# Kernel tuning notes

Hardware: AMD Instinct MI355X
Metric: run time of the kernel (lower is better)

## Reference

```python
import jax, jax.numpy as jnp
import numpy as np

T, B = 256, 512
IMG_FLAT = 25          # 5*5*num_channels
FEAT = 16; LOC = 4; EMB = 4
LSTM_IN = FEAT + LOC + EMB  # 24
H = 128
GRID = 10.0


def _lin(k, out_d, in_d, scale=0.05):
    kw, kb = jax.random.split(k)
    return (jax.random.normal(kw, (out_d, in_d), jnp.float32) * scale,
            jax.random.normal(kb, (out_d,), jnp.float32) * scale)


def setup_inputs() -> dict:
    key = jax.random.key(0)
    ks = jax.random.split(key, 16)
    image = jax.random.uniform(ks[0], (T * B, 5, 5), jnp.float32) * 255.0
    location = jax.random.uniform(ks[1], (T * B, 2), jnp.float32) * GRID
    message = jax.random.normal(ks[2], (T * B, 1), jnp.float32)
    done = jax.random.randint(ks[3], (T * B,), 0, 2, jnp.int32)
    h0 = jnp.zeros((1, B, H), jnp.float32)
    c0 = jnp.zeros((1, B, H), jnp.float32)
    Wv1, bv1 = _lin(ks[4], 256, IMG_FLAT)
    Wv2, bv2 = _lin(ks[5], 256, 256)
    Wv3, bv3 = _lin(ks[6], 128, 256)
    Wv4, bv4 = _lin(ks[7], FEAT, 128)
    Wl, bl = _lin(ks[8], LOC, 2)
    Wm, bm = _lin(ks[9], EMB, 1)
    Wih, bih = _lin(ks[10], 4 * H, LSTM_IN)
    Whh, bhh = _lin(ks[11], 4 * H, H)
    return dict(image=image, location=location, message=message, done=done,
                h0=h0, c0=c0,
                Wv1=Wv1, bv1=bv1, Wv2=Wv2, bv2=bv2, Wv3=Wv3, bv3=bv3,
                Wv4=Wv4, bv4=bv4, Wl=Wl, bl=bl, Wm=Wm, bm=bm,
                Wih=Wih, bih=bih, Whh=Whh, bhh=bhh)


def _get_states(image, location, message, done_f, h0, c0,
                Wv1, bv1, Wv2, bv2, Wv3, bv3, Wv4, bv4,
                Wl, bl, Wm, bm, Wih, bih, Whh, bhh):
    batch = h0.shape[1]
    # encoders (all rows at once, faithful to torch version)
    x = image.reshape(image.shape[0], -1) / 255.0
    f = jax.nn.relu(x @ Wv1.T + bv1)
    f = jax.nn.relu(f @ Wv2.T + bv2)
    f = jax.nn.relu(f @ Wv3.T + bv3)
    image_feat = jax.nn.relu(f @ Wv4.T + bv4)                  # [TB, 16]
    loc_feat = (location / GRID) @ Wl.T + bl                    # [TB, 4]
    msg = (1.0 - done_f)[:, None] * message
    msg_feat = jax.nn.relu(msg @ Wm.T + bm)                     # [TB, 4]
    hid = jnp.concatenate([image_feat, loc_feat, msg_feat], axis=1)
    hid = hid.reshape(-1, batch, LSTM_IN)                       # [T, B, 24]
    d_seq = done_f.reshape(-1, batch)                           # [T, B]

    def step(carry, xd):
        h, c = carry
        x_t, d_t = xd
        mask = (1.0 - d_t)[:, None]
        h = h * mask
        c = c * mask
        gates = x_t @ Wih.T + bih + h @ Whh.T + bhh             # [B, 4H]
        i, fg, g, o = jnp.split(gates, 4, axis=-1)
        c = jax.nn.sigmoid(fg) * c + jax.nn.sigmoid(i) * jnp.tanh(g)
        h = jax.nn.sigmoid(o) * jnp.tanh(c)
        return (h, c), h

    (hT, cT), hs = jax.lax.scan(step, (h0[0], c0[0]), (hid, d_seq))
    new_hidden = hs.reshape(-1, H)                              # [TB, 128]
    return new_hidden, hT[None], cT[None]


def reference(image, location, message, done, h0, c0,
              Wv1, bv1, Wv2, bv2, Wv3, bv3, Wv4, bv4,
              Wl, bl, Wm, bm, Wih, bih, Whh, bhh):
    done_f = done.astype(jnp.float32)
    return _get_states(image, location, message, done_f, h0, c0,
                       Wv1, bv1, Wv2, bv2, Wv3, bv3, Wv4, bv4,
                       Wl, bl, Wm, bm, Wih, bih, Whh, bhh)
```

## Files before the change

### kernel.cpp

```cpp
#include <hip/hip_runtime.h>
#include <hip/hip_bf16.h>

#define T_STEPS 256
#define BATCH   512
#define HID     128
#define TBROWS  (T_STEPS * BATCH)
#define XH_STRIDE 32

typedef short  bh8   __attribute__((ext_vector_type(8)));
typedef _Float16 h8  __attribute__((ext_vector_type(8)));
typedef float  f32x4 __attribute__((ext_vector_type(4)));

__device__ __forceinline__ unsigned short f2bf_bits(float x) {
    union { float f; unsigned int u; } a; a.f = x;
    unsigned int r = a.u + 0x7fffu + ((a.u >> 16) & 1u);
    return (unsigned short)(r >> 16);
}
__device__ __forceinline__ unsigned short f2h_bits(float x) {
    union { _Float16 h; unsigned short u; } z; z.h = (_Float16)x; return z.u;
}
__device__ __forceinline__ unsigned int pack2h(float a, float b) {
    union { _Float16 h[2]; unsigned int u; } z;
    z.h[0] = (_Float16)a; z.h[1] = (_Float16)b; return z.u;
}
__device__ __forceinline__ unsigned int pack2bf(float a, float b) {
    return (unsigned int)f2bf_bits(a) | ((unsigned int)f2bf_bits(b) << 16);
}

#if __has_builtin(__builtin_amdgcn_rcpf)
__device__ __forceinline__ float frcp(float x) { return __builtin_amdgcn_rcpf(x); }
#else
__device__ __forceinline__ float frcp(float x) { return 1.0f / x; }
#endif
#if __has_builtin(__builtin_amdgcn_exp2f)
__device__ __forceinline__ float fexp2(float x) { return __builtin_amdgcn_exp2f(x); }
#else
__device__ __forceinline__ float fexp2(float x) { return __expf(x * 0.6931471806f); }
#endif
#define LOG2E 1.442695041f
__device__ __forceinline__ float sigf(float x) {
    return frcp(1.0f + fexp2(-x * LOG2E));
}
__device__ __forceinline__ float tanh_fast(float x) {
    return fmaf(-2.0f, frcp(1.0f + fexp2(x * (2.0f * LOG2E))), 1.0f);
}

__device__ __forceinline__ float swz16(float v) {
    return __int_as_float(
        __builtin_amdgcn_ds_swizzle(__float_as_int(v), 0x000F));
}

__device__ __forceinline__ void barrier_lds_only() {
    asm volatile("s_waitcnt lgkmcnt(0)" ::: "memory");
    __builtin_amdgcn_s_barrier();
    asm volatile("" ::: "memory");
}

__device__ __forceinline__ void fragstore(unsigned short* dst, const float* W,
                                          int i, int NT, int Kreal) {
    const int j    = i & 7;
    const int lane = (i >> 3) & 63;
    const int ts   = i >> 9;
    const int nt   = ts % NT;
    const int ks   = ts / NT;
    const int n = nt * 16 + (lane & 15);
    const int k = ks * 32 + (lane >> 4) * 8 + j;
    dst[i] = (k < Kreal) ? f2bf_bits(W[n * Kreal + k]) : (unsigned short)0;
}

#define NE1 8192
#define NE2 65536
#define NE3 32768
#define NE4 2048
#define NWC 81920
#define NBS 512
#define PREP_TOTAL (NE1 + NE2 + NE3 + NE4 + NWC + NBS)

__global__ __launch_bounds__(256) void prep_kernel(
    const float* __restrict__ W1, const float* __restrict__ W2,
    const float* __restrict__ W3, const float* __restrict__ W4,
    const float* __restrict__ Wih, const float* __restrict__ bih,
    const float* __restrict__ Whh, const float* __restrict__ bhh,
    unsigned short* __restrict__ w1f, unsigned short* __restrict__ w2f,
    unsigned short* __restrict__ w3f, unsigned short* __restrict__ w4f,
    unsigned short* __restrict__ wcf, float* __restrict__ bsum)
{
    int i = blockIdx.x * 256 + threadIdx.x;
    if (i < NE1) { fragstore(w1f, W1, i, 16, 25); return; }
    i -= NE1;
    if (i < NE2) { fragstore(w2f, W2, i, 16, 256); return; }
    i -= NE2;
    if (i < NE3) { fragstore(w3f, W3, i, 8, 256); return; }
    i -= NE3;
    if (i < NE4) { fragstore(w4f, W4, i, 1, 128); return; }
    i -= NE4;
    if (i < NWC) {
        const int j    = i & 7;
        const int lane = (i >> 3) & 63;
        const int ts   = i >> 9;
        const int mt   = ts / 5;
        const int kt   = ts - mt * 5;
        const int m = mt * 16 + (lane & 15);
        const int k = kt * 32 + (lane >> 4) * 8 + j;
        float v = 0.0f;
        if (k < 128)      v = Whh[m * 128 + k];
        else if (k < 152) v = Wih[m * 24 + (k - 128)];
        wcf[i] = f2h_bits(v);
        return;
    }
    i -= NWC;
    if (i < NBS) bsum[i] = bih[i] + bhh[i];
}

#define ASTRIDE 264
#define ESAMP 64

__global__ __launch_bounds__(256) void encoder_kernel(
    const float* __restrict__ img,
    const float* __restrict__ loc,
    const float* __restrict__ msg,
    const int*   __restrict__ done,
    const float* __restrict__ B1, const float* __restrict__ B2,
    const float* __restrict__ B3, const float* __restrict__ B4,
    const float* __restrict__ Wl, const float* __restrict__ Bl,
    const float* __restrict__ Wm, const float* __restrict__ Bm,
    const unsigned short* __restrict__ w1f, const unsigned short* __restrict__ w2f,
    const unsigned short* __restrict__ w3f, const unsigned short* __restrict__ w4f,
    unsigned short* __restrict__ xcat_h)
{
    __shared__ __align__(16) unsigned short actA[ESAMP][ASTRIDE];
    __shared__ __align__(16) unsigned short actB[ESAMP][ASTRIDE];

    const int tid  = threadIdx.x;
    const int w    = tid >> 6;
    const int lane = tid & 63;
    const int n    = lane & 15;
    const int quad = lane >> 4;
    const int row0 = blockIdx.x * ESAMP;

    if (tid < ESAMP) {
        const int grow = row0 + tid;
        const float l0 = loc[(size_t)grow * 2 + 0] * 0.1f;
        const float l1 = loc[(size_t)grow * 2 + 1] * 0.1f;
        #pragma unroll
        for (int c = 0; c < 4; ++c)
            xcat_h[(size_t)grow * XH_STRIDE + 16 + c] =
                f2h_bits(fmaf(Wl[c * 2 + 0], l0, fmaf(Wl[c * 2 + 1], l1, Bl[c])));
        const float mm = (1.0f - (float)done[grow]) * msg[grow];
        #pragma unroll
        for (int c = 0; c < 4; ++c)
            xcat_h[(size_t)grow * XH_STRIDE + 20 + c] =
                f2h_bits(fmaxf(fmaf(Wm[c], mm, Bm[c]), 0.0f));
    }

    const f32x4 zero4 = {0.0f, 0.0f, 0.0f, 0.0f};

    {
        bh8 bimg[4];
        #pragma unroll
        for (int sg = 0; sg < 4; ++sg) {
            const size_t grow = row0 + sg * 16 + n;
            #pragma unroll
            for (int j = 0; j < 8; ++j) {
                const int k = quad * 8 + j;
                const float v = (k < 25) ? img[grow * 25 + k] * (1.0f / 255.0f) : 0.0f;
                bimg[sg][j] = (short)f2bf_bits(v);
            }
        }
        #pragma unroll
        for (int mt = 0; mt < 4; ++mt) {
            const int mtg = w * 4 + mt;
            const bh8 a = *reinterpret_cast<const bh8*>(w1f + (size_t)(mtg * 64 + lane) * 8);
            f32x4 acc[4];
            #pragma unroll
            for (int sg = 0; sg < 4; ++sg)
                acc[sg] = __builtin_amdgcn_mfma_f32_16x16x32_bf16(a, bimg[sg], zero4, 0, 0, 0);
            const float4 bv = *reinterpret_cast<const float4*>(B1 + mtg * 16 + quad * 4);
            #pragma unroll
            for (int sg = 0; sg < 4; ++sg) {
                const float v0 = fmaxf(acc[sg][0] + bv.x, 0.0f);
                const float v1 = fmaxf(acc[sg][1] + bv.y, 0.0f);
                const float v2 = fmaxf(acc[sg][2] + bv.z, 0.0f);
                const float v3 = fmaxf(acc[sg][3] + bv.w, 0.0f);
                uint2 pk; pk.x = pack2bf(v0, v1); pk.y = pack2bf(v2, v3);
                *reinterpret_cast<uint2*>(&actA[sg * 16 + n][mtg * 16 + quad * 4]) = pk;
            }
        }
    }
    __syncthreads();

    {
        f32x4 a2[4][4];
        #pragma unroll
        for (int mt = 0; mt < 4; ++mt)
            #pragma unroll
            for (int sg = 0; sg < 4; ++sg) a2[mt][sg] = zero4;
        #pragma unroll
        for (int kt = 0; kt < 8; ++kt) {
            bh8 b[4];
            #pragma unroll
            for (int sg = 0; sg < 4; ++sg)
                b[sg] = *reinterpret_cast<const bh8*>(&actA[sg * 16 + n][kt * 32 + quad * 8]);
            #pragma unroll
            for (int mt = 0; mt < 4; ++mt) {
                const int mtg = w * 4 + mt;
                const bh8 a = *reinterpret_cast<const bh8*>(
                    w2f + (size_t)((kt * 16 + mtg) * 64 + lane) * 8);
                #pragma unroll
                for (int sg = 0; sg < 4; ++sg)
                    a2[mt][sg] = __builtin_amdgcn_mfma_f32_16x16x32_bf16(a, b[sg], a2[mt][sg], 0, 0, 0);
            }
        }
        #pragma unroll
        for (int mt = 0; mt < 4; ++mt) {
            const int mtg = w * 4 + mt;
            const float4 bv = *reinterpret_cast<const float4*>(B2 + mtg * 16 + quad * 4);
            #pragma unroll
            for (int sg = 0; sg < 4; ++sg) {
                const float v0 = fmaxf(a2[mt][sg][0] + bv.x, 0.0f);
                const float v1 = fmaxf(a2[mt][sg][1] + bv.y, 0.0f);
                const float v2 = fmaxf(a2[mt][sg][2] + bv.z, 0.0f);
                const float v3 = fmaxf(a2[mt][sg][3] + bv.w, 0.0f);
                uint2 pk; pk.x = pack2bf(v0, v1); pk.y = pack2bf(v2, v3);
                *reinterpret_cast<uint2*>(&actB[sg * 16 + n][mtg * 16 + quad * 4]) = pk;
            }
        }
    }
    __syncthreads();

    {
        f32x4 a3[2][4];
        #pragma unroll
        for (int mt = 0; mt < 2; ++mt)
            #pragma unroll
            for (int sg = 0; sg < 4; ++sg) a3[mt][sg] = zero4;
        #pragma unroll
        for (int kt = 0; kt < 8; ++kt) {
            bh8 b[4];
            #pragma unroll
            for (int sg = 0; sg < 4; ++sg)
                b[sg] = *reinterpret_cast<const bh8*>(&actB[sg * 16 + n][kt * 32 + quad * 8]);
            #pragma unroll
            for (int mt = 0; mt < 2; ++mt) {
                const int mtg = w * 2 + mt;
                const bh8 a = *reinterpret_cast<const bh8*>(
                    w3f + (size_t)((kt * 8 + mtg) * 64 + lane) * 8);
                #pragma unroll
                for (int sg = 0; sg < 4; ++sg)
                    a3[mt][sg] = __builtin_amdgcn_mfma_f32_16x16x32_bf16(a, b[sg], a3[mt][sg], 0, 0, 0);
            }
        }
        #pragma unroll
        for (int mt = 0; mt < 2; ++mt) {
            const int mtg = w * 2 + mt;
            const float4 bv = *reinterpret_cast<const float4*>(B3 + mtg * 16 + quad * 4);
            #pragma unroll
            for (int sg = 0; sg < 4; ++sg) {
                const float v0 = fmaxf(a3[mt][sg][0] + bv.x, 0.0f);
                const float v1 = fmaxf(a3[mt][sg][1] + bv.y, 0.0f);
                const float v2 = fmaxf(a3[mt][sg][2] + bv.z, 0.0f);
                const float v3 = fmaxf(a3[mt][sg][3] + bv.w, 0.0f);
                uint2 pk; pk.x = pack2bf(v0, v1); pk.y = pack2bf(v2, v3);
                *reinterpret_cast<uint2*>(&actA[sg * 16 + n][mtg * 16 + quad * 4]) = pk;
            }
        }
    }
    __syncthreads();

    {
        f32x4 a4 = zero4;
        #pragma unroll
        for (int kt = 0; kt < 4; ++kt) {
            const bh8 b = *reinterpret_cast<const bh8*>(&actA[w * 16 + n][kt * 32 + quad * 8]);
            const bh8 a = *reinterpret_cast<const bh8*>(w4f + (size_t)(kt * 64 + lane) * 8);
            a4 = __builtin_amdgcn_mfma_f32_16x16x32_bf16(a, b, a4, 0, 0, 0);
        }
        const float4 bv = *reinterpret_cast<const float4*>(B4 + quad * 4);
        const int grow = row0 + w * 16 + n;
        const float v0 = fmaxf(a4[0] + bv.x, 0.0f);
        const float v1 = fmaxf(a4[1] + bv.y, 0.0f);
        const float v2 = fmaxf(a4[2] + bv.z, 0.0f);
        const float v3 = fmaxf(a4[3] + bv.w, 0.0f);
        uint2 pk; pk.x = pack2h(v0, v1); pk.y = pack2h(v2, v3);
        *reinterpret_cast<uint2*>(xcat_h + (size_t)grow * XH_STRIDE + quad * 4) = pk;
    }
}

#define COLS 2

__global__ __launch_bounds__(512) void lstm_kernel(
    const unsigned short* __restrict__ xcat_h,
    const int*   __restrict__ done,
    const float* __restrict__ h0,
    const float* __restrict__ c0,
    const unsigned short* __restrict__ wcf,
    const float* __restrict__ bsum,
    float* __restrict__ out)
{
    __shared__ __align__(16) unsigned short xls[T_STEPS][COLS][32];
    __shared__ __align__(16) unsigned short hx[2][COLS][HID];
    __shared__ int dls[T_STEPS][COLS];

    const int tid  = threadIdx.x;
    const int w    = tid >> 6;
    const int lane = tid & 63;
    const int n    = lane & 15;
    const int quad = lane >> 4;
    const int bb   = blockIdx.x * COLS;

    for (int i = tid; i < T_STEPS * COLS * 16; i += 512) {
        const int dw = i & 15;
        const int rc = i >> 4;
        const int st = rc >> 1, cl = rc & 1;
        unsigned int v = 0u;
        if (dw < 12)
            v = *reinterpret_cast<const unsigned int*>(
                xcat_h + (size_t)(st * BATCH + bb + cl) * XH_STRIDE + dw * 2);
        *reinterpret_cast<unsigned int*>(&xls[st][cl][dw * 2]) = v;
    }
    if (tid < T_STEPS * COLS) {
        const int st = tid >> 1, cl = tid & 1;
        dls[st][cl] = done[st * BATCH + bb + cl];
    }

    h8 wf[4][5];
    #pragma unroll
    for (int g = 0; g < 4; ++g)
        #pragma unroll
        for (int kt = 0; kt < 5; ++kt)
            wf[g][kt] = *reinterpret_cast<const h8*>(
                wcf + (size_t)(((g * 8 + w) * 5 + kt) * 64 + lane) * 8);

    const int unit = w * 16 + n;
    f32x4 bini[4];
    #pragma unroll
    for (int g = 0; g < 4; ++g) {
        const float b = bsum[g * 128 + unit];
        bini[g] = (f32x4){b, b, b, b};
    }

    const bool owner = (lane < 32);
    const int col = quad & 1;

    float c_ = 0.0f, h0v = 0.0f;
    if (owner) {
        c_  = c0[(size_t)(bb + col) * HID + unit];
        h0v = h0[(size_t)(bb + col) * HID + unit];
    }
    __syncthreads();

    if (owner)
        hx[0][col][unit] = f2h_bits(h0v * (1.0f - (float)dls[0][col]));
    __syncthreads();

    float hl = 0.0f;

    h8 bf[5];
    #pragma unroll
    for (int kt = 0; kt < 5; ++kt) bf[kt] = (h8)(_Float16)0.0f;

    #pragma unroll 1
    for (int s = 0; s < T_STEPS; ++s) {
        const int buf = s & 1;

        if (n < COLS) {
            #pragma unroll
            for (int kt = 0; kt < 4; ++kt)
                bf[kt] = *reinterpret_cast<const h8*>(&hx[buf][n][kt * 32 + quad * 8]);
            bf[4] = *reinterpret_cast<const h8*>(&xls[s][n][quad * 8]);
        }

        const int sn = (s + 1 < T_STEPS) ? s + 1 : T_STEPS - 1;
        const int m_cur = dls[s][col];
        const int m_nxt = dls[sn][col];

        f32x4 acc[4];
        #pragma unroll
        for (int g = 0; g < 4; ++g) acc[g] = bini[g];
        #pragma unroll
        for (int kt = 0; kt < 5; ++kt)
            #pragma unroll
            for (int g = 0; g < 4; ++g)
                acc[g] = __builtin_amdgcn_mfma_f32_16x16x32_f16(
                    bf[kt], wf[g][kt], acc[g], 0, 0, 0);

        float g4[4];
        #pragma unroll
        for (int g = 0; g < 4; ++g) {
            const float t0 = swz16(acc[g][0]);
            const float t1 = swz16(acc[g][1]);
            g4[g] = (lane & 16) ? t1 : t0;
        }

        if (owner) {
            const float cn = sigf(g4[1]) * (c_ * (1.0f - (float)m_cur))
                           + sigf(g4[0]) * tanh_fast(g4[2]);
            const float hn = sigf(g4[3]) * tanh_fast(cn);
            c_ = cn; hl = hn;
            out[(size_t)(s * BATCH + bb + col) * HID + unit] = hn;
            hx[buf ^ 1][col][unit] = f2h_bits(hn * (1.0f - (float)m_nxt));
        }
        barrier_lds_only();
    }

    const size_t base = (size_t)TBROWS * HID;
    if (owner) {
        out[base + (size_t)(bb + col) * HID + unit] = hl;
        out[base + (size_t)BATCH * HID + (size_t)(bb + col) * HID + unit] = c_;
    }
}

extern "C" void kernel_launch(void* const* d_in, const int* in_sizes, int n_in,
                              void* d_out, int out_size, void* d_ws, size_t ws_size,
                              hipStream_t stream) {
    const float* img  = (const float*)d_in[0];
    const float* loc  = (const float*)d_in[1];
    const float* msg  = (const float*)d_in[2];
    const int*   done = (const int*)d_in[3];
    const float* h0   = (const float*)d_in[4];
    const float* c0   = (const float*)d_in[5];
    const float* W1   = (const float*)d_in[6];
    const float* B1   = (const float*)d_in[7];
    const float* W2   = (const float*)d_in[8];
    const float* B2   = (const float*)d_in[9];
    const float* W3   = (const float*)d_in[10];
    const float* B3   = (const float*)d_in[11];
    const float* W4   = (const float*)d_in[12];
    const float* B4   = (const float*)d_in[13];
    const float* Wl   = (const float*)d_in[14];
    const float* Bl   = (const float*)d_in[15];
    const float* Wm   = (const float*)d_in[16];
    const float* Bm   = (const float*)d_in[17];
    const float* Wih  = (const float*)d_in[18];
    const float* bih  = (const float*)d_in[19];
    const float* Whh  = (const float*)d_in[20];
    const float* bhh  = (const float*)d_in[21];

    char* wsb = (char*)d_ws;
    unsigned short* xcat_h = (unsigned short*)wsb;
    unsigned short* w1f = (unsigned short*)(wsb + (size_t)TBROWS * XH_STRIDE * 2);
    unsigned short* w2f = w1f + NE1;
    unsigned short* w3f = w2f + NE2;
    unsigned short* w4f = w3f + NE3;
    unsigned short* wcf = w4f + NE4;
    float*          bsum = (float*)(wcf + NWC);

    float* out = (float*)d_out;

    prep_kernel<<<(PREP_TOTAL + 255) / 256, 256, 0, stream>>>(
        W1, W2, W3, W4, Wih, bih, Whh, bhh,
        w1f, w2f, w3f, w4f, wcf, bsum);
    encoder_kernel<<<TBROWS / ESAMP, 256, 0, stream>>>(
        img, loc, msg, done, B1, B2, B3, B4, Wl, Bl, Wm, Bm,
        w1f, w2f, w3f, w4f, xcat_h);
    lstm_kernel<<<BATCH / COLS, 512, 0, stream>>>(
        xcat_h, done, h0, c0, wcf, bsum, out);
}
```

Baseline: 344.4 us.

## Make encoder persistent over 8 tiles with register-resident weights and prefetch

The encoder now runs 512-thread blocks that each process 8 tiles of 64 rows. Every wave loads its MFMA weight fragments and biases into registers once, instead of re-reading them from global memory for each 64-row tile. The biases are folded into the accumulator initialisation, and the next tile's image data is prefetched while the current tile computes. The cost is much higher register pressure (launch bounds 512,2), an extra barrier per tile and fewer blocks in the grid. Wave 4 and above sit idle in the last layer.

```diff
diff --git a/kernel.cpp b/kernel.cpp
--- a/kernel.cpp
+++ b/kernel.cpp
@@ -113,9 +113,134 @@
 }
 
 #define ASTRIDE 264
-#define ESAMP 64
-
-__global__ __launch_bounds__(256) void encoder_kernel(
+#define ETILES 8
+#define EBLK   512
+
+__device__ __forceinline__ void enc_tile(
+    const float* __restrict__ img, unsigned short* __restrict__ xcat_h,
+    unsigned short (*bufA)[ASTRIDE], unsigned short (*bufB)[ASTRIDE],
+    const bh8 (&wf1)[2], const bh8 (&wf2)[8][2], const bh8 (&wf3)[8],
+    const bh8 (&wf4)[4],
+    const f32x4 (&bi1)[2], const f32x4 (&bi2)[2], const f32x4& bi3,
+    const f32x4& bi4,
+    float (&fin)[4][8], float (&fnx)[4][8],
+    int row0, int nrow0, bool pf, int w, int n, int quad)
+{
+    bh8 bimg[4];
+    #pragma unroll
+    for (int sg = 0; sg < 4; ++sg)
+        #pragma unroll
+        for (int j = 0; j < 8; ++j)
+            bimg[sg][j] = (short)f2bf_bits(fin[sg][j] * (1.0f / 255.0f));
+
+    if (pf) {
+        #pragma unroll
+        for (int sg = 0; sg < 4; ++sg) {
+            const size_t grow = (size_t)(nrow0 + sg * 16 + n);
+            #pragma unroll
+            for (int j = 0; j < 8; ++j) {
+                const int k = quad * 8 + j;
+                fnx[sg][j] = (k < 25) ? img[grow * 25 + k] : 0.0f;
+            }
+        }
+    }
+
+    #pragma unroll
+    for (int mt = 0; mt < 2; ++mt) {
+        f32x4 acc[4];
+        #pragma unroll
+        for (int sg = 0; sg < 4; ++sg)
+            acc[sg] = __builtin_amdgcn_mfma_f32_16x16x32_bf16(
+                wf1[mt], bimg[sg], bi1[mt], 0, 0, 0);
+        #pragma unroll
+        for (int sg = 0; sg < 4; ++sg) {
+            uint2 pk;
+            pk.x = pack2bf(fmaxf(acc[sg][0], 0.0f), fmaxf(acc[sg][1], 0.0f));
+            pk.y = pack2bf(fmaxf(acc[sg][2], 0.0f), fmaxf(acc[sg][3], 0.0f));
+            *reinterpret_cast<uint2*>(
+                &bufA[sg * 16 + n][(2 * w + mt) * 16 + quad * 4]) = pk;
+        }
+    }
+    barrier_lds_only();
+
+    {
+        f32x4 a2[2][4];
+        #pragma unroll
+        for (int mt = 0; mt < 2; ++mt)
+            #pragma unroll
+            for (int sg = 0; sg < 4; ++sg) a2[mt][sg] = bi2[mt];
+        #pragma unroll
+        for (int kt = 0; kt < 8; ++kt) {
+            bh8 b[4];
+            #pragma unroll
+            for (int sg = 0; sg < 4; ++sg)
+                b[sg] = *reinterpret_cast<const bh8*>(
+                    &bufA[sg * 16 + n][kt * 32 + quad * 8]);
+            #pragma unroll
+            for (int mt = 0; mt < 2; ++mt)
+                #pragma unroll
+                for (int sg = 0; sg < 4; ++sg)
+                    a2[mt][sg] = __builtin_amdgcn_mfma_f32_16x16x32_bf16(
+                        wf2[kt][mt], b[sg], a2[mt][sg], 0, 0, 0);
+        }
+        #pragma unroll
+        for (int mt = 0; mt < 2; ++mt)
+            #pragma unroll
+            for (int sg = 0; sg < 4; ++sg) {
+                uint2 pk;
+                pk.x = pack2bf(fmaxf(a2[mt][sg][0], 0.0f), fmaxf(a2[mt][sg][1], 0.0f));
+                pk.y = pack2bf(fmaxf(a2[mt][sg][2], 0.0f), fmaxf(a2[mt][sg][3], 0.0f));
+                *reinterpret_cast<uint2*>(
+                    &bufB[sg * 16 + n][(2 * w + mt) * 16 + quad * 4]) = pk;
+            }
+    }
+    barrier_lds_only();
+
+    {
+        f32x4 a3[4];
+        #pragma unroll
+        for (int sg = 0; sg < 4; ++sg) a3[sg] = bi3;
+        #pragma unroll
+        for (int kt = 0; kt < 8; ++kt) {
+            bh8 b[4];
+            #pragma unroll
+            for (int sg = 0; sg < 4; ++sg)
+                b[sg] = *reinterpret_cast<const bh8*>(
+                    &bufB[sg * 16 + n][kt * 32 + quad * 8]);
+            #pragma unroll
+            for (int sg = 0; sg < 4; ++sg)
+                a3[sg] = __builtin_amdgcn_mfma_f32_16x16x32_bf16(
+                    wf3[kt], b[sg], a3[sg], 0, 0, 0);
+        }
+        #pragma unroll
+        for (int sg = 0; sg < 4; ++sg) {
+            uint2 pk;
+            pk.x = pack2bf(fmaxf(a3[sg][0], 0.0f), fmaxf(a3[sg][1], 0.0f));
+            pk.y = pack2bf(fmaxf(a3[sg][2], 0.0f), fmaxf(a3[sg][3], 0.0f));
+            *reinterpret_cast<uint2*>(
+                &bufA[sg * 16 + n][w * 16 + quad * 4]) = pk;
+        }
+    }
+    barrier_lds_only();
+
+    if (w < 4) {
+        f32x4 a4 = bi4;
+        #pragma unroll
+        for (int kt = 0; kt < 4; ++kt) {
+            const bh8 b = *reinterpret_cast<const bh8*>(
+                &bufA[w * 16 + n][kt * 32 + quad * 8]);
+            a4 = __builtin_amdgcn_mfma_f32_16x16x32_bf16(wf4[kt], b, a4, 0, 0, 0);
+        }
+        const int grow = row0 + w * 16 + n;
+        uint2 pk;
+        pk.x = pack2h(fmaxf(a4[0], 0.0f), fmaxf(a4[1], 0.0f));
+        pk.y = pack2h(fmaxf(a4[2], 0.0f), fmaxf(a4[3], 0.0f));
+        *reinterpret_cast<uint2*>(xcat_h + (size_t)grow * XH_STRIDE + quad * 4) = pk;
+    }
+    barrier_lds_only();
+}
+
+__global__ __launch_bounds__(512, 2) void encoder_kernel(
     const float* __restrict__ img,
     const float* __restrict__ loc,
     const float* __restrict__ msg,
@@ -128,18 +253,18 @@
     const unsigned short* __restrict__ w3f, const unsigned short* __restrict__ w4f,
     unsigned short* __restrict__ xcat_h)
 {
-    __shared__ __align__(16) unsigned short actA[ESAMP][ASTRIDE];
-    __shared__ __align__(16) unsigned short actB[ESAMP][ASTRIDE];
+    __shared__ __align__(16) unsigned short bufA[64][ASTRIDE];
+    __shared__ __align__(16) unsigned short bufB[64][ASTRIDE];
 
     const int tid  = threadIdx.x;
     const int w    = tid >> 6;
     const int lane = tid & 63;
     const int n    = lane & 15;
     const int quad = lane >> 4;
-    const int row0 = blockIdx.x * ESAMP;
-
-    if (tid < ESAMP) {
-        const int grow = row0 + tid;
+    const int blk0 = blockIdx.x * EBLK;
+
+    {
+        const int grow = blk0 + tid;
         const float l0 = loc[(size_t)grow * 2 + 0] * 0.1f;
         const float l1 = loc[(size_t)grow * 2 + 1] * 0.1f;
         #pragma unroll
@@ -153,136 +278,61 @@
                 f2h_bits(fmaxf(fmaf(Wm[c], mm, Bm[c]), 0.0f));
     }
 
-    const f32x4 zero4 = {0.0f, 0.0f, 0.0f, 0.0f};
-
+    float fA[4][8], fB[4][8];
+    #pragma unroll
+    for (int sg = 0; sg < 4; ++sg) {
+        const size_t grow = (size_t)(blk0 + sg * 16 + n);
+        #pragma unroll
+        for (int j = 0; j < 8; ++j) {
+            const int k = quad * 8 + j;
+            fA[sg][j] = (k < 25) ? img[grow * 25 + k] : 0.0f;
+        }
+    }
+
+    bh8 wf1[2], wf2[8][2], wf3[8], wf4[4];
+    #pragma unroll
+    for (int mt = 0; mt < 2; ++mt)
+        wf1[mt] = *reinterpret_cast<const bh8*>(
+            w1f + (size_t)((2 * w + mt) * 64 + lane) * 8);
+    #pragma unroll
+    for (int kt = 0; kt < 8; ++kt)
+        #pragma unroll
+        for (int mt = 0; mt < 2; ++mt)
+            wf2[kt][mt] = *reinterpret_cast<const bh8*>(
+                w2f + (size_t)((kt * 16 + 2 * w + mt) * 64 + lane) * 8);
+    #pragma unroll
+    for (int kt = 0; kt < 8; ++kt)
+        wf3[kt] = *reinterpret_cast<const bh8*>(
+            w3f + (size_t)((kt * 8 + w) * 64 + lane) * 8);
+    #pragma unroll
+    for (int kt = 0; kt < 4; ++kt)
+        wf4[kt] = *reinterpret_cast<const bh8*>(
+            w4f + (size_t)(kt * 64 + lane) * 8);
+
+    f32x4 bi1[2], bi2[2], bi3, bi4;
+    #pragma unroll
+    for (int mt = 0; mt < 2; ++mt) {
+        float4 v = *reinterpret_cast<const float4*>(B1 + (2 * w + mt) * 16 + quad * 4);
+        bi1[mt] = (f32x4){v.x, v.y, v.z, v.w};
+        float4 u = *reinterpret_cast<const float4*>(B2 + (2 * w + mt) * 16 + quad * 4);
+        bi2[mt] = (f32x4){u.x, u.y, u.z, u.w};
+    }
     {
-        bh8 bimg[4];
-        #pragma unroll
-        for (int sg = 0; sg < 4; ++sg) {
-            const size_t grow = row0 + sg * 16 + n;
-            #pragma unroll
-            for (int j = 0; j < 8; ++j) {
-                const int k = quad * 8 + j;
-                const float v = (k < 25) ? img[grow * 25 + k] * (1.0f / 255.0f) : 0.0f;
-                bimg[sg][j] = (short)f2bf_bits(v);
-            }
-        }
-        #pragma unroll
-        for (int mt = 0; mt < 4; ++mt) {
-            const int mtg = w * 4 + mt;
-            const bh8 a = *reinterpret_cast<const bh8*>(w1f + (size_t)(mtg * 64 + lane) * 8);
-            f32x4 acc[4];
-            #pragma unroll
-            for (int sg = 0; sg < 4; ++sg)
-                acc[sg] = __builtin_amdgcn_mfma_f32_16x16x32_bf16(a, bimg[sg], zero4, 0, 0, 0);
-            const float4 bv = *reinterpret_cast<const float4*>(B1 + mtg * 16 + quad * 4);
-            #pragma unroll
-            for (int sg = 0; sg < 4; ++sg) {
-                const float v0 = fmaxf(acc[sg][0] + bv.x, 0.0f);
-                const float v1 = fmaxf(acc[sg][1] + bv.y, 0.0f);
-                const float v2 = fmaxf(acc[sg][2] + bv.z, 0.0f);
-                const float v3 = fmaxf(acc[sg][3] + bv.w, 0.0f);
-                uint2 pk; pk.x = pack2bf(v0, v1); pk.y = pack2bf(v2, v3);
-                *reinterpret_cast<uint2*>(&actA[sg * 16 + n][mtg * 16 + quad * 4]) = pk;
-            }
-        }
-    }
-    __syncthreads();
-
-    {
-        f32x4 a2[4][4];
-        #pragma unroll
-        for (int mt = 0; mt < 4; ++mt)
-            #pragma unroll
-            for (int sg = 0; sg < 4; ++sg) a2[mt][sg] = zero4;
-        #pragma unroll
-        for (int kt = 0; kt < 8; ++kt) {
-            bh8 b[4];
-            #pragma unroll
-            for (int sg = 0; sg < 4; ++sg)
-                b[sg] = *reinterpret_cast<const bh8*>(&actA[sg * 16 + n][kt * 32 + quad * 8]);
-            #pragma unroll
-            for (int mt = 0; mt < 4; ++mt) {
-                const int mtg = w * 4 + mt;
-                const bh8 a = *reinterpret_cast<const bh8*>(
-                    w2f + (size_t)((kt * 16 + mtg) * 64 + lane) * 8);
-                #pragma unroll
-                for (int sg = 0; sg < 4; ++sg)
-                    a2[mt][sg] = __builtin_amdgcn_mfma_f32_16x16x32_bf16(a, b[sg], a2[mt][sg], 0, 0, 0);
-            }
-        }
-        #pragma unroll
-        for (int mt = 0; mt < 4; ++mt) {
-            const int mtg = w * 4 + mt;
-            const float4 bv = *reinterpret_cast<const float4*>(B2 + mtg * 16 + quad * 4);
-            #pragma unroll
-            for (int sg = 0; sg < 4; ++sg) {
-                const float v0 = fmaxf(a2[mt][sg][0] + bv.x, 0.0f);
-                const float v1 = fmaxf(a2[mt][sg][1] + bv.y, 0.0f);
-                const float v2 = fmaxf(a2[mt][sg][2] + bv.z, 0.0f);
-                const float v3 = fmaxf(a2[mt][sg][3] + bv.w, 0.0f);
-                uint2 pk; pk.x = pack2bf(v0, v1); pk.y = pack2bf(v2, v3);
-                *reinterpret_cast<uint2*>(&actB[sg * 16 + n][mtg * 16 + quad * 4]) = pk;
-            }
-        }
-    }
-    __syncthreads();
-
-    {
-        f32x4 a3[2][4];
-        #pragma unroll
-        for (int mt = 0; mt < 2; ++mt)
-            #pragma unroll
-            for (int sg = 0; sg < 4; ++sg) a3[mt][sg] = zero4;
-        #pragma unroll
-        for (int kt = 0; kt < 8; ++kt) {
-            bh8 b[4];
-            #pragma unroll
-            for (int sg = 0; sg < 4; ++sg)
-                b[sg] = *reinterpret_cast<const bh8*>(&actB[sg * 16 + n][kt * 32 + quad * 8]);
-            #pragma unroll
-            for (int mt = 0; mt < 2; ++mt) {
-                const int mtg = w * 2 + mt;
-                const bh8 a = *reinterpret_cast<const bh8*>(
-                    w3f + (size_t)((kt * 8 + mtg) * 64 + lane) * 8);
-                #pragma unroll
-                for (int sg = 0; sg < 4; ++sg)
-                    a3[mt][sg] = __builtin_amdgcn_mfma_f32_16x16x32_bf16(a, b[sg], a3[mt][sg], 0, 0, 0);
-            }
-        }
-        #pragma unroll
-        for (int mt = 0; mt < 2; ++mt) {
-            const int mtg = w * 2 + mt;
-            const float4 bv = *reinterpret_cast<const float4*>(B3 + mtg * 16 + quad * 4);
-            #pragma unroll
-            for (int sg = 0; sg < 4; ++sg) {
-                const float v0 = fmaxf(a3[mt][sg][0] + bv.x, 0.0f);
-                const float v1 = fmaxf(a3[mt][sg][1] + bv.y, 0.0f);
-                const float v2 = fmaxf(a3[mt][sg][2] + bv.z, 0.0f);
-                const float v3 = fmaxf(a3[mt][sg][3] + bv.w, 0.0f);
-                uint2 pk; pk.x = pack2bf(v0, v1); pk.y = pack2bf(v2, v3);
-                *reinterpret_cast<uint2*>(&actA[sg * 16 + n][mtg * 16 + quad * 4]) = pk;
-            }
-        }
-    }
-    __syncthreads();
-
-    {
-        f32x4 a4 = zero4;
-        #pragma unroll
-        for (int kt = 0; kt < 4; ++kt) {
-            const bh8 b = *reinterpret_cast<const bh8*>(&actA[w * 16 + n][kt * 32 + quad * 8]);
-            const bh8 a = *reinterpret_cast<const bh8*>(w4f + (size_t)(kt * 64 + lane) * 8);
-            a4 = __builtin_amdgcn_mfma_f32_16x16x32_bf16(a, b, a4, 0, 0, 0);
-        }
-        const float4 bv = *reinterpret_cast<const float4*>(B4 + quad * 4);
-        const int grow = row0 + w * 16 + n;
-        const float v0 = fmaxf(a4[0] + bv.x, 0.0f);
-        const float v1 = fmaxf(a4[1] + bv.y, 0.0f);
-        const float v2 = fmaxf(a4[2] + bv.z, 0.0f);
-        const float v3 = fmaxf(a4[3] + bv.w, 0.0f);
-        uint2 pk; pk.x = pack2h(v0, v1); pk.y = pack2h(v2, v3);
-        *reinterpret_cast<uint2*>(xcat_h + (size_t)grow * XH_STRIDE + quad * 4) = pk;
+        float4 v = *reinterpret_cast<const float4*>(B3 + w * 16 + quad * 4);
+        bi3 = (f32x4){v.x, v.y, v.z, v.w};
+        float4 u = *reinterpret_cast<const float4*>(B4 + quad * 4);
+        bi4 = (f32x4){u.x, u.y, u.z, u.w};
+    }
+
+    #pragma unroll 1
+    for (int t = 0; t < ETILES; t += 2) {
+        enc_tile(img, xcat_h, bufA, bufB, wf1, wf2, wf3, wf4,
+                 bi1, bi2, bi3, bi4, fA, fB,
+                 blk0 + t * 64, blk0 + (t + 1) * 64, true, w, n, quad);
+        enc_tile(img, xcat_h, bufA, bufB, wf1, wf2, wf3, wf4,
+                 bi1, bi2, bi3, bi4, fB, fA,
+                 blk0 + (t + 1) * 64, blk0 + (t + 2) * 64, t + 2 < ETILES,
+                 w, n, quad);
     }
 }
 
@@ -450,7 +500,7 @@
     prep_kernel<<<(PREP_TOTAL + 255) / 256, 256, 0, stream>>>(
         W1, W2, W3, W4, Wih, bih, Whh, bhh,
         w1f, w2f, w3f, w4f, wcf, bsum);
-    encoder_kernel<<<TBROWS / ESAMP, 256, 0, stream>>>(
+    encoder_kernel<<<TBROWS / EBLK, 512, 0, stream>>>(
         img, loc, msg, done, B1, B2, B3, B4, Wl, Bl, Wm, Bm,
         w1f, w2f, w3f, w4f, xcat_h);
     lstm_kernel<<<BATCH / COLS, 512, 0, stream>>>(
```

Measured after the change: 362.5 us. +5.3%, slower.

## Split encoder work across 8 waves and stage image rows in LDS

Applied to the files above, without the earlier changes.

The encoder block grows from 4 to 8 wavefronts. Each wave now computes half as many output tiles in layers 1-3, and only the first 4 waves run the final layer. Image rows are loaded cooperatively and coalesced into shared memory before being converted to bf16 MFMA operands, replacing strided per-lane global loads. The aim is lower accumulator register pressure, higher occupancy and better latency hiding. The cost is an extra barrier, more LDS per block, and idle waves during layer 4.

```diff
diff --git a/kernel.cpp b/kernel.cpp
--- a/kernel.cpp
+++ b/kernel.cpp
@@ -115,7 +115,7 @@
 #define ASTRIDE 264
 #define ESAMP 64
 
-__global__ __launch_bounds__(256) void encoder_kernel(
+__global__ __launch_bounds__(512, 4) void encoder_kernel(
     const float* __restrict__ img,
     const float* __restrict__ loc,
     const float* __restrict__ msg,
@@ -128,6 +128,7 @@
     const unsigned short* __restrict__ w3f, const unsigned short* __restrict__ w4f,
     unsigned short* __restrict__ xcat_h)
 {
+    __shared__ float imgLS[ESAMP][26];
     __shared__ __align__(16) unsigned short actA[ESAMP][ASTRIDE];
     __shared__ __align__(16) unsigned short actB[ESAMP][ASTRIDE];
 
@@ -138,6 +139,9 @@
     const int quad = lane >> 4;
     const int row0 = blockIdx.x * ESAMP;
 
+    for (int i = tid; i < ESAMP * 25; i += 512)
+        imgLS[i / 25][i % 25] = img[(size_t)row0 * 25 + i];
+
     if (tid < ESAMP) {
         const int grow = row0 + tid;
         const float l0 = loc[(size_t)grow * 2 + 0] * 0.1f;
@@ -152,24 +156,23 @@
             xcat_h[(size_t)grow * XH_STRIDE + 20 + c] =
                 f2h_bits(fmaxf(fmaf(Wm[c], mm, Bm[c]), 0.0f));
     }
+    __syncthreads();
 
     const f32x4 zero4 = {0.0f, 0.0f, 0.0f, 0.0f};
 
     {
         bh8 bimg[4];
         #pragma unroll
-        for (int sg = 0; sg < 4; ++sg) {
-            const size_t grow = row0 + sg * 16 + n;
+        for (int sg = 0; sg < 4; ++sg)
             #pragma unroll
             for (int j = 0; j < 8; ++j) {
                 const int k = quad * 8 + j;
-                const float v = (k < 25) ? img[grow * 25 + k] * (1.0f / 255.0f) : 0.0f;
+                const float v = (k < 25) ? imgLS[sg * 16 + n][k] * (1.0f / 255.0f) : 0.0f;
                 bimg[sg][j] = (short)f2bf_bits(v);
             }
-        }
-        #pragma unroll
-        for (int mt = 0; mt < 4; ++mt) {
-            const int mtg = w * 4 + mt;
+        #pragma unroll
+        for (int mt = 0; mt < 2; ++mt) {
+            const int mtg = 2 * w + mt;
             const bh8 a = *reinterpret_cast<const bh8*>(w1f + (size_t)(mtg * 64 + lane) * 8);
             f32x4 acc[4];
             #pragma unroll
@@ -190,9 +193,9 @@
     __syncthreads();
 
     {
-        f32x4 a2[4][4];
-        #pragma unroll
-        for (int mt = 0; mt < 4; ++mt)
+        f32x4 a2[2][4];
+        #pragma unroll
+        for (int mt = 0; mt < 2; ++mt)
             #pragma unroll
             for (int sg = 0; sg < 4; ++sg) a2[mt][sg] = zero4;
         #pragma unroll
@@ -202,8 +205,8 @@
             for (int sg = 0; sg < 4; ++sg)
                 b[sg] = *reinterpret_cast<const bh8*>(&actA[sg * 16 + n][kt * 32 + quad * 8]);
             #pragma unroll
-            for (int mt = 0; mt < 4; ++mt) {
-                const int mtg = w * 4 + mt;
+            for (int mt = 0; mt < 2; ++mt) {
+                const int mtg = 2 * w + mt;
                 const bh8 a = *reinterpret_cast<const bh8*>(
                     w2f + (size_t)((kt * 16 + mtg) * 64 + lane) * 8);
                 #pragma unroll
@@ -212,8 +215,8 @@
             }
         }
         #pragma unroll
-        for (int mt = 0; mt < 4; ++mt) {
-            const int mtg = w * 4 + mt;
+        for (int mt = 0; mt < 2; ++mt) {
+            const int mtg = 2 * w + mt;
             const float4 bv = *reinterpret_cast<const float4*>(B2 + mtg * 16 + quad * 4);
             #pragma unroll
             for (int sg = 0; sg < 4; ++sg) {
@@ -229,45 +232,35 @@
     __syncthreads();
 
     {
-        f32x4 a3[2][4];
-        #pragma unroll
-        for (int mt = 0; mt < 2; ++mt)
-            #pragma unroll
-            for (int sg = 0; sg < 4; ++sg) a3[mt][sg] = zero4;
+        f32x4 a3[4];
+        #pragma unroll
+        for (int sg = 0; sg < 4; ++sg) a3[sg] = zero4;
         #pragma unroll
         for (int kt = 0; kt < 8; ++kt) {
             bh8 b[4];
             #pragma unroll
             for (int sg = 0; sg < 4; ++sg)
                 b[sg] = *reinterpret_cast<const bh8*>(&actB[sg * 16 + n][kt * 32 + quad * 8]);
-            #pragma unroll
-            for (int mt = 0; mt < 2; ++mt) {
-                const int mtg = w * 2 + mt;
-                const bh8 a = *reinterpret_cast<const bh8*>(
-                    w3f + (size_t)((kt * 8 + mtg) * 64 + lane) * 8);
-                #pragma unroll
-                for (int sg = 0; sg < 4; ++sg)
-                    a3[mt][sg] = __builtin_amdgcn_mfma_f32_16x16x32_bf16(a, b[sg], a3[mt][sg], 0, 0, 0);
-            }
-        }
-        #pragma unroll
-        for (int mt = 0; mt < 2; ++mt) {
-            const int mtg = w * 2 + mt;
-            const float4 bv = *reinterpret_cast<const float4*>(B3 + mtg * 16 + quad * 4);
-            #pragma unroll
-            for (int sg = 0; sg < 4; ++sg) {
-                const float v0 = fmaxf(a3[mt][sg][0] + bv.x, 0.0f);
-                const float v1 = fmaxf(a3[mt][sg][1] + bv.y, 0.0f);
-                const float v2 = fmaxf(a3[mt][sg][2] + bv.z, 0.0f);
-                const float v3 = fmaxf(a3[mt][sg][3] + bv.w, 0.0f);
-                uint2 pk; pk.x = pack2bf(v0, v1); pk.y = pack2bf(v2, v3);
-                *reinterpret_cast<uint2*>(&actA[sg * 16 + n][mtg * 16 + quad * 4]) = pk;
-            }
-        }
-    }
-    __syncthreads();
-
-    {
+            const bh8 a = *reinterpret_cast<const bh8*>(
+                w3f + (size_t)((kt * 8 + w) * 64 + lane) * 8);
+            #pragma unroll
+            for (int sg = 0; sg < 4; ++sg)
+                a3[sg] = __builtin_amdgcn_mfma_f32_16x16x32_bf16(a, b[sg], a3[sg], 0, 0, 0);
+        }
+        const float4 bv = *reinterpret_cast<const float4*>(B3 + w * 16 + quad * 4);
+        #pragma unroll
+        for (int sg = 0; sg < 4; ++sg) {
+            const float v0 = fmaxf(a3[sg][0] + bv.x, 0.0f);
+            const float v1 = fmaxf(a3[sg][1] + bv.y, 0.0f);
+            const float v2 = fmaxf(a3[sg][2] + bv.z, 0.0f);
+            const float v3 = fmaxf(a3[sg][3] + bv.w, 0.0f);
+            uint2 pk; pk.x = pack2bf(v0, v1); pk.y = pack2bf(v2, v3);
+            *reinterpret_cast<uint2*>(&actA[sg * 16 + n][w * 16 + quad * 4]) = pk;
+        }
+    }
+    __syncthreads();
+
+    if (w < 4) {
         f32x4 a4 = zero4;
         #pragma unroll
         for (int kt = 0; kt < 4; ++kt) {
@@ -450,7 +443,7 @@
     prep_kernel<<<(PREP_TOTAL + 255) / 256, 256, 0, stream>>>(
         W1, W2, W3, W4, Wih, bih, Whh, bhh,
         w1f, w2f, w3f, w4f, wcf, bsum);
-    encoder_kernel<<<TBROWS / ESAMP, 256, 0, stream>>>(
+    encoder_kernel<<<TBROWS / ESAMP, 512, 0, stream>>>(
         img, loc, msg, done, B1, B2, B3, B4, Wl, Bl, Wm, Bm,
         w1f, w2f, w3f, w4f, xcat_h);
     lstm_kernel<<<BATCH / COLS, 512, 0, stream>>>(
```

After: 336.7 us. 2.2% less time.
